# Performance work log

Measured on AMD Instinct MI355X. Metric: run time of the kernel, lower is better.

Reference implementation:

```python
import jax, jax.numpy as jnp
from jax import lax
import numpy as np

T, B = 64, 32            # rollout length, num envs
IMG = 84                 # NatureCNN input size
POS_N = 10               # grid size per position axis
N_ACT = 5                # discrete actions
HID = 128                # LSTM hidden size
CNN_OUT = 512
IN_DIM = CNN_OUT + 2 * POS_N  # 532


def setup_inputs() -> dict:
    key = jax.random.key(0)
    ks = jax.random.split(key, 16)
    N = T * B
    s = 0.05  # weight scale to keep activations in sane range
    rn = lambda k, shp: jax.random.normal(k, shp, jnp.float32) * s
    return {
        "image": jax.random.uniform(ks[0], (N, IMG, IMG, 3), jnp.float32),
        "position": jax.random.randint(ks[1], (N, 2), 0, POS_N, jnp.int32),
        "done": jax.random.randint(ks[2], (N,), 0, 2, jnp.int32),
        "h0": jnp.zeros((B, 1, HID), jnp.float32),
        "c0": jnp.zeros((B, 1, HID), jnp.float32),
        "W1": rn(ks[3], (8, 8, 3, 32)),   "b1": jnp.zeros((32,), jnp.float32),
        "W2": rn(ks[4], (4, 4, 32, 64)),  "b2": jnp.zeros((64,), jnp.float32),
        "W3": rn(ks[5], (3, 3, 64, 64)),  "b3": jnp.zeros((64,), jnp.float32),
        "Wfc": rn(ks[6], (3136, CNN_OUT)), "bfc": jnp.zeros((CNN_OUT,), jnp.float32),
        "Wih": rn(ks[7], (4 * HID, IN_DIM)), "Whh": rn(ks[8], (4 * HID, HID)),
        "bih": jnp.zeros((4 * HID,), jnp.float32), "bhh": jnp.zeros((4 * HID,), jnp.float32),
        "Wp": rn(ks[9], (HID, N_ACT)), "bp": jnp.zeros((N_ACT,), jnp.float32),
        "Wv": rn(ks[10], (HID, 1)),    "bv": jnp.zeros((1,), jnp.float32),
    }


def _conv(x, w, b, stride):
    y = lax.conv_general_dilated(x, w, (stride, stride), 'VALID',
                                 dimension_numbers=('NHWC', 'HWIO', 'NHWC'))
    return jax.nn.relu(y + b)


def reference(image, position, done, h0, c0,
              W1, b1, W2, b2, W3, b3, Wfc, bfc,
              Wih, Whh, bih, bhh, Wp, bp, Wv, bv):
    # --- NatureCNN feature extractor ---
    x = _conv(image, W1, b1, 4)          # (N,20,20,32)
    x = _conv(x, W2, b2, 2)              # (N,9,9,64)
    x = _conv(x, W3, b3, 1)              # (N,7,7,64)
    x = x.reshape(x.shape[0], -1)        # (N,3136)
    feat = jax.nn.relu(x @ Wfc + bfc)    # (N,512)
    # --- one-hot position encoding ---
    oh = jnp.concatenate([jax.nn.one_hot(position[:, 0], POS_N, dtype=feat.dtype),
                          jax.nn.one_hot(position[:, 1], POS_N, dtype=feat.dtype)], axis=1)
    z = jnp.concatenate([feat, oh], axis=1).reshape(T, B, IN_DIM)
    d = done.astype(feat.dtype).reshape(T, B)
    # --- per-timestep masked LSTM scan with episode resets ---
    h = h0[:, 0, :]  # (B,HID), num_layers=1
    c = c0[:, 0, :]

    def step(carry, inp):
        h, c = carry
        x_t, d_t = inp
        m = (1.0 - d_t)[:, None]
        h = h * m
        c = c * m
        g = x_t @ Wih.T + bih + h @ Whh.T + bhh          # (B,4*HID)
        i, f, gg, o = jnp.split(g, 4, axis=1)             # torch gate order i,f,g,o
        i = jax.nn.sigmoid(i)
        f = jax.nn.sigmoid(f)
        o = jax.nn.sigmoid(o)
        c = f * c + i * jnp.tanh(gg)
        h = o * jnp.tanh(c)
        return (h, c), h

    (h, c), hs = lax.scan(step, (h, c), (z, d))
    H = hs.reshape(T * B, HID)
    logits = H @ Wp + bp                 # (N, N_ACT) -> Categorical logits
    v = H @ Wv + bv                      # (N, 1)
    return logits, v, h[:, None, :], c[:, None, :]
```

## Files before the change

kernel.cpp:

```cpp
#include <hip/hip_runtime.h>

typedef unsigned short ushort_t;
typedef unsigned int uint_t;
typedef __attribute__((ext_vector_type(8))) short short8;
typedef __attribute__((ext_vector_type(4))) short short4v;
typedef __attribute__((ext_vector_type(4))) float floatx4;

__device__ __forceinline__ float bf2f(ushort_t u){
    union { uint_t i; float f; } c; c.i = ((uint_t)u) << 16; return c.f;
}
__device__ __forceinline__ ushort_t f2bf(float x){
    union { float f; uint_t i; } c; c.f = x;
    uint_t i = c.i;
    return (ushort_t)((i + 0x7fffu + ((i >> 16) & 1u)) >> 16);
}
__device__ __forceinline__ uint_t cvt2fast(float a, float b){
    union { float f; uint_t i; } ca, cb; ca.f = a; cb.f = b;
    uint_t ia = ca.i + 0x8000u, ib = cb.i + 0x8000u;
    return __builtin_amdgcn_perm(ib, ia, 0x07060302u);
}
__device__ __forceinline__ float relu_f(float x){ return fmaxf(x, 0.0f); }
__device__ __forceinline__ float sigmoid_f(float x){ return 1.0f / (1.0f + __expf(-x)); }

#define NT 2048
#define TT 64

__global__ __launch_bounds__(256) void prep_kernel(
    const float* __restrict__ Wih, ushort_t* __restrict__ Wihb)
{
    int i = blockIdx.x * 256 + threadIdx.x;
    int j = i >> 9, k = i & 511;
    Wihb[i] = f2bf(Wih[j * 532 + k]);
}

__global__ __launch_bounds__(256) void prep_convw_kernel(
    const float* __restrict__ W1, const float* __restrict__ W2,
    const float* __restrict__ W3, ushort_t* __restrict__ W1b,
    ushort_t* __restrict__ W2b, ushort_t* __restrict__ W3b)
{
    int i = blockIdx.x * 256 + threadIdx.x;
    if (i < 8192) {
        int ky = i >> 10, oc = (i >> 5) & 31, k = i & 31;
        float v = 0.0f;
        if (k < 24) { int kx = k / 3, ic = k % 3; v = W1[((ky * 8 + kx) * 3 + ic) * 32 + oc]; }
        W1b[i] = f2bf(v);
        return;
    }
    i -= 8192;
    if (i < 32768) {
        int kk = i >> 11, oc = (i >> 5) & 63, ic = i & 31;
        W2b[i] = f2bf(W2[(kk * 32 + ic) * 64 + oc]);
        return;
    }
    i -= 32768;
    if (i < 36864) {
        int p = i >> 12, oc = (i >> 6) & 63, ic = i & 63;
        W3b[i] = f2bf(W3[(p * 64 + ic) * 64 + oc]);
    }
}

__global__ __launch_bounds__(256) void wfct_kernel(
    const float* __restrict__ Wfc, ushort_t* __restrict__ WfcT)
{
    __shared__ ushort_t t_s[64][65];
    int kb = blockIdx.x % 49, jb = blockIdx.x / 49;
    int k0 = kb * 64, j0 = jb * 64;
    int jj = threadIdx.x & 63, i4 = threadIdx.x >> 6;
    for (int rr = i4; rr < 64; rr += 4)
        t_s[rr][jj] = f2bf(Wfc[(size_t)(k0 + rr) * 512 + j0 + jj]);
    __syncthreads();
    for (int rr = i4; rr < 64; rr += 4)
        WfcT[(size_t)(j0 + rr) * 3136 + k0 + jj] = t_s[jj][rr];
}

__global__ __launch_bounds__(256, 4) void convs_mfma(
    const float* __restrict__ img,
    const ushort_t* __restrict__ W1b, const float* __restrict__ b1,
    const ushort_t* __restrict__ W2b, const float* __restrict__ b2,
    const ushort_t* __restrict__ W3b, const float* __restrict__ b3,
    ushort_t* __restrict__ out3)
{
    __shared__ __align__(16) ushort_t smem[12864];

    int n = blockIdx.x, tid = threadIdx.x;
    int w = tid >> 6, lane = tid & 63;
    int r = lane & 15, q = lane >> 4;

    {
        short8 bf0[8], bf1[8];
        #pragma unroll
        for (int ky = 0; ky < 8; ky++) {
            bf0[ky] = *(const short8*)(W1b + (ky * 32 +      r) * 32 + q * 8);
            bf1[ky] = *(const short8*)(W1b + (ky * 32 + 16 + r) * 32 + q * 8);
        }
        float bb0 = b1[r], bb1 = b1[16 + r];
        const float* abase = img + (size_t)n * 21168;

        int t = w;
        for (; t + 4 < 25; t += 8) {
            int pxaA = t * 16 + r, pxaB = (t + 4) * 16 + r;
            int oyA = pxaA / 20, oxA = pxaA % 20;
            int oyB = pxaB / 20, oxB = pxaB % 20;
            floatx4 aA0 = {0.f,0.f,0.f,0.f}, aA1 = {0.f,0.f,0.f,0.f};
            floatx4 aB0 = {0.f,0.f,0.f,0.f}, aB1 = {0.f,0.f,0.f,0.f};
            #pragma unroll
            for (int ky = 0; ky < 8; ky++) {
                short8 a = {0,0,0,0,0,0,0,0};
                short8 b = {0,0,0,0,0,0,0,0};
                if (q < 3) {
                    const float* pA = abase + ((oyA * 4 + ky) * 84 + oxA * 4) * 3 + q * 8;
                    const float* pB = abase + ((oyB * 4 + ky) * 84 + oxB * 4) * 3 + q * 8;
                    float4 fA0 = *(const float4*)pA;
                    float4 fA1 = *(const float4*)(pA + 4);
                    float4 fB0 = *(const float4*)pB;
                    float4 fB1 = *(const float4*)(pB + 4);
                    union { uint_t u[4]; short8 s; } pk;
                    pk.u[0] = cvt2fast(fA0.x, fA0.y);
                    pk.u[1] = cvt2fast(fA0.z, fA0.w);
                    pk.u[2] = cvt2fast(fA1.x, fA1.y);
                    pk.u[3] = cvt2fast(fA1.z, fA1.w);
                    a = pk.s;
                    pk.u[0] = cvt2fast(fB0.x, fB0.y);
                    pk.u[1] = cvt2fast(fB0.z, fB0.w);
                    pk.u[2] = cvt2fast(fB1.x, fB1.y);
                    pk.u[3] = cvt2fast(fB1.z, fB1.w);
                    b = pk.s;
                }
                aA0 = __builtin_amdgcn_mfma_f32_16x16x32_bf16(a, bf0[ky], aA0, 0, 0, 0);
                aA1 = __builtin_amdgcn_mfma_f32_16x16x32_bf16(a, bf1[ky], aA1, 0, 0, 0);
                aB0 = __builtin_amdgcn_mfma_f32_16x16x32_bf16(b, bf0[ky], aB0, 0, 0, 0);
                aB1 = __builtin_amdgcn_mfma_f32_16x16x32_bf16(b, bf1[ky], aB1, 0, 0, 0);
            }
            #pragma unroll
            for (int pair = 0; pair < 2; pair++) {
                int tt = t + pair * 4;
                floatx4 acc0 = pair ? aB0 : aA0;
                floatx4 acc1 = pair ? aB1 : aA1;
                int pxs = tt * 16 + q * 4;
                #pragma unroll
                for (int i = 0; i < 4; i++) {
                    int px = pxs + i;
                    int y = px / 20, x = px % 20;
                    int base = (x & 1) * 4 * 1608 + (y * 10 + (x >> 1)) * 8 + (r & 7);
                    smem[base + ((r >> 3)    ) * 1608] = f2bf(relu_f(acc0[i] + bb0));
                    smem[base + (2 + (r >> 3)) * 1608] = f2bf(relu_f(acc1[i] + bb1));
                }
            }
        }
        if (t < 25) {
            int pxa = t * 16 + r;
            int oy = pxa / 20, ox = pxa % 20;
            floatx4 acc0 = {0.f,0.f,0.f,0.f}, acc1 = {0.f,0.f,0.f,0.f};
            #pragma unroll
            for (int ky = 0; ky < 8; ky++) {
                short8 a = {0,0,0,0,0,0,0,0};
                if (q < 3) {
                    const float* p = abase + ((oy * 4 + ky) * 84 + ox * 4) * 3 + q * 8;
                    float4 f0 = *(const float4*)p;
                    float4 f1 = *(const float4*)(p + 4);
                    union { uint_t u[4]; short8 s; } pk;
                    pk.u[0] = cvt2fast(f0.x, f0.y);
                    pk.u[1] = cvt2fast(f0.z, f0.w);
                    pk.u[2] = cvt2fast(f1.x, f1.y);
                    pk.u[3] = cvt2fast(f1.z, f1.w);
                    a = pk.s;
                }
                acc0 = __builtin_amdgcn_mfma_f32_16x16x32_bf16(a, bf0[ky], acc0, 0, 0, 0);
                acc1 = __builtin_amdgcn_mfma_f32_16x16x32_bf16(a, bf1[ky], acc1, 0, 0, 0);
            }
            int pxs = t * 16 + q * 4;
            #pragma unroll
            for (int i = 0; i < 4; i++) {
                int px = pxs + i;
                int y = px / 20, x = px % 20;
                int base = (x & 1) * 4 * 1608 + (y * 10 + (x >> 1)) * 8 + (r & 7);
                smem[base + ((r >> 3)    ) * 1608] = f2bf(relu_f(acc0[i] + bb0));
                smem[base + (2 + (r >> 3)) * 1608] = f2bf(relu_f(acc1[i] + bb1));
            }
        }
    }
    __syncthreads();

    float accv[6][4];
    {
        int oct = w;
        short8 bfr[16];
        #pragma unroll
        for (int kk = 0; kk < 16; kk++)
            bfr[kk] = *(const short8*)(W2b + (kk * 64 + oct * 16 + r) * 32 + q * 8);
        #pragma unroll
        for (int t = 0; t < 6; t++) {
            int pxa = min(t * 16 + r, 80);
            int oy = pxa / 9, ox = pxa % 9;
            floatx4 acc = {0.f, 0.f, 0.f, 0.f};
            #pragma unroll
            for (int ky = 0; ky < 4; ky++) {
                #pragma unroll
                for (int kxh = 0; kxh < 2; kxh++) {
                    int pos = (oy * 2 + ky) * 10 + ox + kxh;
                    const ushort_t* pe = smem + q * 1608 + pos * 8;
                    short8 ae = *(const short8*)pe;
                    short8 ao = *(const short8*)(pe + 4 * 1608);
                    acc = __builtin_amdgcn_mfma_f32_16x16x32_bf16(ae, bfr[ky * 4 + kxh * 2],     acc, 0, 0, 0);
                    acc = __builtin_amdgcn_mfma_f32_16x16x32_bf16(ao, bfr[ky * 4 + kxh * 2 + 1], acc, 0, 0, 0);
                }
            }
            #pragma unroll
            for (int i = 0; i < 4; i++) accv[t][i] = acc[i];
        }
    }
    __syncthreads();
    {
        int oct = w;
        float bb = b2[oct * 16 + r];
        int kcb = (oct * 2 + (r >> 3)) * 656 + (r & 7);
        #pragma unroll
        for (int t = 0; t < 6; t++) {
            #pragma unroll
            for (int i = 0; i < 4; i++) {
                int px = t * 16 + q * 4 + i;
                if (px < 81)
                    smem[kcb + px * 8] = f2bf(relu_f(accv[t][i] + bb));
            }
        }
    }
    __syncthreads();

    {
        int oct = w;
        short8 bfr[18];
        #pragma unroll
        for (int p = 0; p < 9; p++) {
            #pragma unroll
            for (int h = 0; h < 2; h++)
                bfr[p * 2 + h] = *(const short8*)(W3b + (p * 64 + oct * 16 + r) * 64 + h * 32 + q * 8);
        }
        float bb = b3[oct * 16 + r];
        for (int t = 0; t < 4; t++) {
            int pxa = min(t * 16 + r, 48);
            int oy = pxa / 7, ox = pxa % 7;
            floatx4 acc = {0.f, 0.f, 0.f, 0.f};
            #pragma unroll
            for (int ky = 0; ky < 3; ky++) {
                #pragma unroll
                for (int kx = 0; kx < 3; kx++) {
                    int qin = (oy + ky) * 9 + ox + kx;
                    const ushort_t* p0 = smem + q * 656 + qin * 8;
                    short8 a0 = *(const short8*)p0;
                    short8 a1 = *(const short8*)(p0 + 4 * 656);
                    acc = __builtin_amdgcn_mfma_f32_16x16x32_bf16(a0, bfr[(ky * 3 + kx) * 2],     acc, 0, 0, 0);
                    acc = __builtin_amdgcn_mfma_f32_16x16x32_bf16(a1, bfr[(ky * 3 + kx) * 2 + 1], acc, 0, 0, 0);
                }
            }
            #pragma unroll
            for (int i = 0; i < 4; i++) {
                int px = t * 16 + q * 4 + i;
                if (px < 49)
                    out3[(size_t)n * 3136 + px * 64 + oct * 16 + r] = f2bf(relu_f(acc[i] + bb));
            }
        }
    }
}

__global__ __launch_bounds__(256) void fc_mfma_kernel(
    const ushort_t* __restrict__ A, const ushort_t* __restrict__ BT,
    const float* __restrict__ bfc, ushort_t* __restrict__ feat)
{
    int mb = blockIdx.x & 63, nb = blockIdx.x >> 6;
    int tid = threadIdx.x;
    int w = tid >> 6, lane = tid & 63;
    int r = lane & 15, q = lane >> 4;
    int m0 = mb * 32 + (w & 1) * 16;
    int n0 = nb * 64 + (w >> 1) * 32;
    const ushort_t* arow  = A  + (size_t)(m0 + r) * 3136 + q * 8;
    const ushort_t* brow0 = BT + (size_t)(n0 + r) * 3136 + q * 8;
    const ushort_t* brow1 = BT + (size_t)(n0 + 16 + r) * 3136 + q * 8;
    floatx4 acc0 = {0.f, 0.f, 0.f, 0.f}, acc1 = {0.f, 0.f, 0.f, 0.f};
    short8 a  = *(const short8*)arow;
    short8 b0 = *(const short8*)brow0;
    short8 b1 = *(const short8*)brow1;
    for (int kk = 1; kk < 98; kk++) {
        short8 an  = *(const short8*)(arow  + kk * 32);
        short8 b0n = *(const short8*)(brow0 + kk * 32);
        short8 b1n = *(const short8*)(brow1 + kk * 32);
        acc0 = __builtin_amdgcn_mfma_f32_16x16x32_bf16(a, b0, acc0, 0, 0, 0);
        acc1 = __builtin_amdgcn_mfma_f32_16x16x32_bf16(a, b1, acc1, 0, 0, 0);
        a = an; b0 = b0n; b1 = b1n;
    }
    acc0 = __builtin_amdgcn_mfma_f32_16x16x32_bf16(a, b0, acc0, 0, 0, 0);
    acc1 = __builtin_amdgcn_mfma_f32_16x16x32_bf16(a, b1, acc1, 0, 0, 0);
    int c0 = n0 + r, c1 = n0 + 16 + r;
    float bb0 = bfc[c0], bb1 = bfc[c1];
    #pragma unroll
    for (int i = 0; i < 4; i++) {
        int row = m0 + q * 4 + i;
        feat[(size_t)row * 512 + c0] = f2bf(relu_f(acc0[i] + bb0));
        feat[(size_t)row * 512 + c1] = f2bf(relu_f(acc1[i] + bb1));
    }
}

__global__ __launch_bounds__(256) void gates_mfma_kernel(
    const ushort_t* __restrict__ A, const ushort_t* __restrict__ Wihb,
    const float* __restrict__ Wih, const float* __restrict__ bih,
    const float* __restrict__ bhh, const int* __restrict__ pos,
    float* __restrict__ gx)
{
    int mb = blockIdx.x & 63, nb = blockIdx.x >> 6;
    int tid = threadIdx.x;
    int w = tid >> 6, lane = tid & 63;
    int r = lane & 15, q = lane >> 4;
    int m0 = mb * 32 + (w & 1) * 16;
    int n0 = nb * 64 + (w >> 1) * 32;
    const ushort_t* arow  = A    + (size_t)(m0 + r) * 512 + q * 8;
    const ushort_t* brow0 = Wihb + (size_t)(n0 + r) * 512 + q * 8;
    const ushort_t* brow1 = Wihb + (size_t)(n0 + 16 + r) * 512 + q * 8;
    floatx4 acc0 = {0.f, 0.f, 0.f, 0.f}, acc1 = {0.f, 0.f, 0.f, 0.f};
    short8 a  = *(const short8*)arow;
    short8 b0 = *(const short8*)brow0;
    short8 b1 = *(const short8*)brow1;
    for (int kk = 1; kk < 16; kk++) {
        short8 an  = *(const short8*)(arow  + kk * 32);
        short8 b0n = *(const short8*)(brow0 + kk * 32);
        short8 b1n = *(const short8*)(brow1 + kk * 32);
        acc0 = __builtin_amdgcn_mfma_f32_16x16x32_bf16(a, b0, acc0, 0, 0, 0);
        acc1 = __builtin_amdgcn_mfma_f32_16x16x32_bf16(a, b1, acc1, 0, 0, 0);
        a = an; b0 = b0n; b1 = b1n;
    }
    acc0 = __builtin_amdgcn_mfma_f32_16x16x32_bf16(a, b0, acc0, 0, 0, 0);
    acc1 = __builtin_amdgcn_mfma_f32_16x16x32_bf16(a, b1, acc1, 0, 0, 0);
    int j0 = n0 + r, j1 = n0 + 16 + r;
    float bias0 = bih[j0] + bhh[j0];
    float bias1 = bih[j1] + bhh[j1];
    #pragma unroll
    for (int i = 0; i < 4; i++) {
        int row = m0 + q * 4 + i;
        int p0 = pos[2 * row], p1 = pos[2 * row + 1];
        float oh0 = Wih[(size_t)j0 * 532 + 512 + p0] + Wih[(size_t)j0 * 532 + 522 + p1];
        float oh1 = Wih[(size_t)j1 * 532 + 512 + p0] + Wih[(size_t)j1 * 532 + 522 + p1];
        gx[(size_t)row * 512 + j0] = acc0[i] + bias0 + oh0;
        gx[(size_t)row * 512 + j1] = acc1[i] + bias1 + oh1;
    }
}

__global__ __launch_bounds__(512, 2) void lstm_kernel(
    const float* __restrict__ gx, const float* __restrict__ Whh,
    const int* __restrict__ done, const float* __restrict__ h0,
    const float* __restrict__ c0, ushort_t* __restrict__ hs,
    float* __restrict__ out)
{
    __shared__ __align__(16) float h_s[128];
    __shared__ float gates_s[512];
    int b = blockIdx.x, tid = threadIdx.x;
    int g = tid >> 7, j = tid & 127;

    float w[128];
    const float* wr = Whh + (size_t)(g * 128 + j) * 128;
    #pragma unroll
    for (int k = 0; k < 128; k += 4) {
        float4 v = *(const float4*)(wr + k);
        w[k] = v.x; w[k + 1] = v.y; w[k + 2] = v.z; w[k + 3] = v.w;
    }
    float h = h0[b * 128 + j];
    float c = c0[b * 128 + j];
    const float* gxb = gx + (size_t)b * 512;

    for (int t = 0; t < TT; t++) {
        float m = 1.0f - (float)done[t * 32 + b];
        c *= m;
        if (g == 0) h_s[j] = h * m;
        __syncthreads();
        float acc = 0.0f;
        #pragma unroll
        for (int k = 0; k < 128; k += 4) {
            float4 hv = *(const float4*)&h_s[k];
            acc = fmaf(w[k], hv.x, acc);
            acc = fmaf(w[k + 1], hv.y, acc);
            acc = fmaf(w[k + 2], hv.z, acc);
            acc = fmaf(w[k + 3], hv.w, acc);
        }
        acc += gxb[(size_t)t * 32 * 512 + (g << 7) + j];
        gates_s[(g << 7) + j] = acc;
        __syncthreads();
        float iv = sigmoid_f(gates_s[j]);
        float fv = sigmoid_f(gates_s[128 + j]);
        float gv = tanhf(gates_s[256 + j]);
        float ov = sigmoid_f(gates_s[384 + j]);
        c = fv * c + iv * gv;
        h = ov * tanhf(c);
        if (g == 0) hs[((size_t)t * 32 + b) * 128 + j] = f2bf(h);
    }
    if (g == 0) {
        out[12288 + b * 128 + j] = h;
        out[16384 + b * 128 + j] = c;
    }
}

__global__ __launch_bounds__(256) void heads_kernel(
    const ushort_t* __restrict__ hs, const float* __restrict__ Wp,
    const float* __restrict__ bp, const float* __restrict__ Wv,
    const float* __restrict__ bv, float* __restrict__ out)
{
    int id = blockIdx.x * 256 + threadIdx.x;
    int n = id / 6, q = id % 6;
    const ushort_t* hrow = hs + (size_t)n * 128;
    if (q < 5) {
        float acc = bp[q];
        for (int k = 0; k < 128; k++) acc = fmaf(bf2f(hrow[k]), Wp[k * 5 + q], acc);
        out[n * 5 + q] = acc;
    } else {
        float acc = bv[0];
        for (int k = 0; k < 128; k++) acc = fmaf(bf2f(hrow[k]), Wv[k], acc);
        out[10240 + n] = acc;
    }
}

extern "C" void kernel_launch(void* const* d_in, const int* in_sizes, int n_in,
                              void* d_out, int out_size, void* d_ws, size_t ws_size,
                              hipStream_t stream) {
    const float* image = (const float*)d_in[0];
    const int*   pos   = (const int*)d_in[1];
    const int*   done  = (const int*)d_in[2];
    const float* h0    = (const float*)d_in[3];
    const float* c0    = (const float*)d_in[4];
    const float* W1    = (const float*)d_in[5];
    const float* b1    = (const float*)d_in[6];
    const float* W2    = (const float*)d_in[7];
    const float* b2    = (const float*)d_in[8];
    const float* W3    = (const float*)d_in[9];
    const float* b3    = (const float*)d_in[10];
    const float* Wfc   = (const float*)d_in[11];
    const float* bfc   = (const float*)d_in[12];
    const float* Wih   = (const float*)d_in[13];
    const float* Whh   = (const float*)d_in[14];
    const float* bih   = (const float*)d_in[15];
    const float* bhh   = (const float*)d_in[16];
    const float* Wp    = (const float*)d_in[17];
    const float* bp    = (const float*)d_in[18];
    const float* Wv    = (const float*)d_in[19];
    const float* bv    = (const float*)d_in[20];

    char* ws = (char*)d_ws;
    ushort_t* Wihb = (ushort_t*)(ws + 0);
    ushort_t* WfcT = (ushort_t*)(ws + 524288);
    ushort_t* W1b  = (ushort_t*)(ws + 3735552);
    ushort_t* W2b  = (ushort_t*)(ws + 3751936);
    ushort_t* W3b  = (ushort_t*)(ws + 3817472);
    ushort_t* out3 = (ushort_t*)(ws + 4194304);
    ushort_t* feat = (ushort_t*)(ws + 17039360);
    float*    gx   = (float*)(ws + 19136512);
    ushort_t* hs   = (ushort_t*)(ws + 23330816);

    float* out = (float*)d_out;

    prep_kernel<<<1024, 256, 0, stream>>>(Wih, Wihb);
    prep_convw_kernel<<<304, 256, 0, stream>>>(W1, W2, W3, W1b, W2b, W3b);
    wfct_kernel<<<392, 256, 0, stream>>>(Wfc, WfcT);
    convs_mfma<<<2048, 256, 0, stream>>>(image, W1b, b1, W2b, b2, W3b, b3, out3);
    fc_mfma_kernel<<<512, 256, 0, stream>>>(out3, WfcT, bfc, feat);
    gates_mfma_kernel<<<512, 256, 0, stream>>>(feat, Wihb, Wih, bih, bhh, pos, gx);
    lstm_kernel<<<32, 512, 0, stream>>>(gx, Whh, done, h0, c0, hs, out);
    heads_kernel<<<48, 256, 0, stream>>>(hs, Wp, bp, Wv, bv, out);
}
```

Baseline: 517.5 us.

## Merge weight-prep kernels, fuse heads into LSTM, prefetch gate inputs

```diff
diff --git a/kernel.cpp b/kernel.cpp
--- a/kernel.cpp
+++ b/kernel.cpp
@@ -25,52 +25,55 @@
 #define NT 2048
 #define TT 64
 
-__global__ __launch_bounds__(256) void prep_kernel(
-    const float* __restrict__ Wih, ushort_t* __restrict__ Wihb)
-{
-    int i = blockIdx.x * 256 + threadIdx.x;
-    int j = i >> 9, k = i & 511;
-    Wihb[i] = f2bf(Wih[j * 532 + k]);
-}
-
-__global__ __launch_bounds__(256) void prep_convw_kernel(
+__global__ __launch_bounds__(256) void prep_all(
+    const float* __restrict__ Wih, ushort_t* __restrict__ Wihb,
     const float* __restrict__ W1, const float* __restrict__ W2,
     const float* __restrict__ W3, ushort_t* __restrict__ W1b,
-    ushort_t* __restrict__ W2b, ushort_t* __restrict__ W3b)
-{
-    int i = blockIdx.x * 256 + threadIdx.x;
-    if (i < 8192) {
-        int ky = i >> 10, oc = (i >> 5) & 31, k = i & 31;
-        float v = 0.0f;
-        if (k < 24) { int kx = k / 3, ic = k % 3; v = W1[((ky * 8 + kx) * 3 + ic) * 32 + oc]; }
-        W1b[i] = f2bf(v);
-        return;
-    }
-    i -= 8192;
-    if (i < 32768) {
-        int kk = i >> 11, oc = (i >> 5) & 63, ic = i & 31;
-        W2b[i] = f2bf(W2[(kk * 32 + ic) * 64 + oc]);
-        return;
-    }
-    i -= 32768;
-    if (i < 36864) {
-        int p = i >> 12, oc = (i >> 6) & 63, ic = i & 63;
-        W3b[i] = f2bf(W3[(p * 64 + ic) * 64 + oc]);
-    }
-}
-
-__global__ __launch_bounds__(256) void wfct_kernel(
+    ushort_t* __restrict__ W2b, ushort_t* __restrict__ W3b,
     const float* __restrict__ Wfc, ushort_t* __restrict__ WfcT)
 {
     __shared__ ushort_t t_s[64][65];
-    int kb = blockIdx.x % 49, jb = blockIdx.x / 49;
-    int k0 = kb * 64, j0 = jb * 64;
-    int jj = threadIdx.x & 63, i4 = threadIdx.x >> 6;
-    for (int rr = i4; rr < 64; rr += 4)
-        t_s[rr][jj] = f2bf(Wfc[(size_t)(k0 + rr) * 512 + j0 + jj]);
-    __syncthreads();
-    for (int rr = i4; rr < 64; rr += 4)
-        WfcT[(size_t)(j0 + rr) * 3136 + k0 + jj] = t_s[jj][rr];
+    int bid = blockIdx.x;
+    if (bid < 1024) {
+        int i = bid * 256 + threadIdx.x;
+        int j = i >> 9, k = i & 511;
+        Wihb[i] = f2bf(Wih[j * 532 + k]);
+        return;
+    }
+    bid -= 1024;
+    if (bid < 304) {
+        int i = bid * 256 + threadIdx.x;
+        if (i < 8192) {
+            int ky = i >> 10, oc = (i >> 5) & 31, k = i & 31;
+            float v = 0.0f;
+            if (k < 24) { int kx = k / 3, ic = k % 3; v = W1[((ky * 8 + kx) * 3 + ic) * 32 + oc]; }
+            W1b[i] = f2bf(v);
+            return;
+        }
+        i -= 8192;
+        if (i < 32768) {
+            int kk = i >> 11, oc = (i >> 5) & 63, ic = i & 31;
+            W2b[i] = f2bf(W2[(kk * 32 + ic) * 64 + oc]);
+            return;
+        }
+        i -= 32768;
+        if (i < 36864) {
+            int p = i >> 12, oc = (i >> 6) & 63, ic = i & 63;
+            W3b[i] = f2bf(W3[(p * 64 + ic) * 64 + oc]);
+        }
+        return;
+    }
+    bid -= 304;
+    {
+        int kb = bid % 49, jb = bid / 49;
+        int k0 = kb * 64, j0 = jb * 64;
+        int jj = threadIdx.x & 63, i4 = threadIdx.x >> 6;
+        for (int rr = i4; rr < 64; rr += 4)
+            t_s[rr][jj] = f2bf(Wfc[(size_t)(k0 + rr) * 512 + j0 + jj]);
+        __syncthreads();
+        for (int rr = i4; rr < 64; rr += 4)
+            WfcT[(size_t)(j0 + rr) * 3136 + k0 + jj] = t_s[jj][rr];
+    }
 }
 
 __global__ __launch_bounds__(256, 4) void convs_mfma(
@@ -78,11 +81,11 @@
     const ushort_t* __restrict__ W1b, const float* __restrict__ b1,
     const ushort_t* __restrict__ W2b, const float* __restrict__ b2,
     const ushort_t* __restrict__ W3b, const float* __restrict__ b3,
-    ushort_t* __restrict__ out3)
+    ushort_t* __restrict__ out3, int nbase)
 {
     __shared__ __align__(16) ushort_t smem[12864];
 
-    int n = blockIdx.x, tid = threadIdx.x;
+    int n = nbase + blockIdx.x, tid = threadIdx.x;
     int w = tid >> 6, lane = tid & 63;
     int r = lane & 15, q = lane >> 4;
 
@@ -345,11 +348,13 @@
 __global__ __launch_bounds__(512, 2) void lstm_kernel(
     const float* __restrict__ gx, const float* __restrict__ Whh,
     const int* __restrict__ done, const float* __restrict__ h0,
-    const float* __restrict__ c0, ushort_t* __restrict__ hs,
-    float* __restrict__ out)
+    const float* __restrict__ c0, const float* __restrict__ Wp,
+    const float* __restrict__ bp, const float* __restrict__ Wv,
+    const float* __restrict__ bv, float* __restrict__ out)
 {
     __shared__ __align__(16) float h_s[128];
     __shared__ float gates_s[512];
+    __shared__ ushort_t hs_s[TT * 132];
     int b = blockIdx.x, tid = threadIdx.x;
     int g = tid >> 7, j = tid & 127;
 
@@ -364,22 +369,23 @@
     float c = c0[b * 128 + j];
     const float* gxb = gx + (size_t)b * 512;
 
+    float gcur = gxb[(g << 7) + j];
     for (int t = 0; t < TT; t++) {
         float m = 1.0f - (float)done[t * 32 + b];
         c *= m;
         if (g == 0) h_s[j] = h * m;
         __syncthreads();
-        float acc = 0.0f;
+        float gnxt = (t + 1 < TT) ? gxb[(size_t)(t + 1) * 32 * 512 + (g << 7) + j] : 0.0f;
+        float a0 = 0.0f, a1 = 0.0f, a2 = 0.0f, a3 = 0.0f;
         #pragma unroll
         for (int k = 0; k < 128; k += 4) {
             float4 hv = *(const float4*)&h_s[k];
-            acc = fmaf(w[k], hv.x, acc);
-            acc = fmaf(w[k + 1], hv.y, acc);
-            acc = fmaf(w[k + 2], hv.z, acc);
-            acc = fmaf(w[k + 3], hv.w, acc);
-        }
-        acc += gxb[(size_t)t * 32 * 512 + (g << 7) + j];
-        gates_s[(g << 7) + j] = acc;
+            a0 = fmaf(w[k],     hv.x, a0);
+            a1 = fmaf(w[k + 1], hv.y, a1);
+            a2 = fmaf(w[k + 2], hv.z, a2);
+            a3 = fmaf(w[k + 3], hv.w, a3);
+        }
+        gates_s[(g << 7) + j] = (a0 + a1) + (a2 + a3) + gcur;
         __syncthreads();
         float iv = sigmoid_f(gates_s[j]);
         float fv = sigmoid_f(gates_s[128 + j]);
@@ -387,30 +393,27 @@
         float ov = sigmoid_f(gates_s[384 + j]);
         c = fv * c + iv * gv;
         h = ov * tanhf(c);
-        if (g == 0) hs[((size_t)t * 32 + b) * 128 + j] = f2bf(h);
+        if (g == 0) hs_s[t * 132 + j] = f2bf(h);
+        gcur = gnxt;
     }
     if (g == 0) {
         out[12288 + b * 128 + j] = h;
         out[16384 + b * 128 + j] = c;
     }
-}
-
-__global__ __launch_bounds__(256) void heads_kernel(
-    const ushort_t* __restrict__ hs, const float* __restrict__ Wp,
-    const float* __restrict__ bp, const float* __restrict__ Wv,
-    const float* __restrict__ bv, float* __restrict__ out)
-{
-    int id = blockIdx.x * 256 + threadIdx.x;
-    int n = id / 6, q = id % 6;
-    const ushort_t* hrow = hs + (size_t)n * 128;
-    if (q < 5) {
-        float acc = bp[q];
-        for (int k = 0; k < 128; k++) acc = fmaf(bf2f(hrow[k]), Wp[k * 5 + q], acc);
-        out[n * 5 + q] = acc;
-    } else {
-        float acc = bv[0];
-        for (int k = 0; k < 128; k++) acc = fmaf(bf2f(hrow[k]), Wv[k], acc);
-        out[10240 + n] = acc;
+    __syncthreads();
+
+    if (tid < TT * 6) {
+        int t = tid / 6, qq = tid % 6;
+        const ushort_t* hr = hs_s + t * 132;
+        if (qq < 5) {
+            float acc = bp[qq];
+            for (int k = 0; k < 128; k++) acc = fmaf(bf2f(hr[k]), Wp[k * 5 + qq], acc);
+            out[(t * 32 + b) * 5 + qq] = acc;
+        } else {
+            float acc = bv[0];
+            for (int k = 0; k < 128; k++) acc = fmaf(bf2f(hr[k]), Wv[k], acc);
+            out[10240 + t * 32 + b] = acc;
+        }
     }
 }
 
@@ -448,16 +451,13 @@
     ushort_t* out3 = (ushort_t*)(ws + 4194304);
     ushort_t* feat = (ushort_t*)(ws + 17039360);
     float*    gx   = (float*)(ws + 19136512);
-    ushort_t* hs   = (ushort_t*)(ws + 23330816);
 
     float* out = (float*)d_out;
 
-    prep_kernel<<<1024, 256, 0, stream>>>(Wih, Wihb);
-    prep_convw_kernel<<<304, 256, 0, stream>>>(W1, W2, W3, W1b, W2b, W3b);
-    wfct_kernel<<<392, 256, 0, stream>>>(Wfc, WfcT);
-    convs_mfma<<<2048, 256, 0, stream>>>(image, W1b, b1, W2b, b2, W3b, b3, out3);
+    prep_all<<<1720, 256, 0, stream>>>(Wih, Wihb, W1, W2, W3, W1b, W2b, W3b, Wfc, WfcT);
+    convs_mfma<<<1024, 256, 0, stream>>>(image, W1b, b1, W2b, b2, W3b, b3, out3, 0);
+    convs_mfma<<<1024, 256, 0, stream>>>(image, W1b, b1, W2b, b2, W3b, b3, out3, 1024);
     fc_mfma_kernel<<<512, 256, 0, stream>>>(out3, WfcT, bfc, feat);
     gates_mfma_kernel<<<512, 256, 0, stream>>>(feat, Wihb, Wih, bih, bhh, pos, gx);
-    lstm_kernel<<<32, 512, 0, stream>>>(gx, Whh, done, h0, c0, hs, out);
-    heads_kernel<<<48, 256, 0, stream>>>(hs, Wp, bp, Wv, bv, out);
-}
+    lstm_kernel<<<32, 512, 0, stream>>>(gx, Whh, done, h0, c0, Wp, bp, Wv, bv, out);
+}
```

After: 554.7 us. +7.2%, slower.
